# Optimization experiments

Measured on AMD Instinct MI355X. Metric: run time of the kernel, lower is better.

The kernel has to match this reference:

```python
import jax, jax.numpy as jnp
import numpy as np

D_MODEL = 1024
N_HEADS = 16
D_K = D_MODEL // N_HEADS
B, S = 2, 2048


def setup_inputs() -> dict:
    key = jax.random.key(0)
    ks = jax.random.split(key, 5)
    sc = 1.0 / np.sqrt(D_MODEL)
    return {
        "x": jax.random.normal(ks[0], (B, S, D_MODEL), dtype=jnp.float32),
        "W_qkv": jax.random.normal(ks[1], (D_MODEL, 3 * D_MODEL), dtype=jnp.float32) * sc,
        "b_qkv": jnp.zeros((3 * D_MODEL,), dtype=jnp.float32),
        "W_out": jax.random.normal(ks[2], (D_MODEL, D_MODEL), dtype=jnp.float32) * sc,
        "b_out": jnp.zeros((D_MODEL,), dtype=jnp.float32),
    }


def reference(x, W_qkv, b_qkv, W_out, b_out):
    Bb, Ss, _ = x.shape
    qkv = x @ W_qkv + b_qkv                     # [B,S,3*D]
    qkv = qkv.reshape(Bb, Ss, 3, N_HEADS, D_K)
    qkv = jnp.transpose(qkv, (2, 0, 3, 1, 4))   # [3,B,H,S,Dk]
    q, k, v = qkv[0], qkv[1], qkv[2]
    scale = jnp.asarray(np.sqrt(D_K), dtype=x.dtype)
    attn = jnp.einsum('bhsd,bhtd->bhst', q, k) / scale  # [B,H,S,S]
    attn = jax.nn.softmax(attn, axis=-1)
    out = jnp.einsum('bhst,bhtd->bhsd', attn, v)        # [B,H,S,Dk]
    out = jnp.transpose(out, (0, 2, 1, 3)).reshape(Bb, Ss, D_MODEL)
    return out @ W_out + b_out
```

## Files before the change

kernel.cpp:

```cpp
#include <hip/hip_runtime.h>

typedef __bf16 bf16x8 __attribute__((ext_vector_type(8)));
typedef __bf16 bf16x4 __attribute__((ext_vector_type(4)));
typedef float f32x4 __attribute__((ext_vector_type(4)));
typedef unsigned short u16;
typedef unsigned int u32;

__device__ __forceinline__ u16 f2bu(float f) {
  __bf16 h = (__bf16)f;
  return __builtin_bit_cast(u16, h);
}

__device__ __forceinline__ void gld16(const u16* g, const __bf16* lds) {
  __builtin_amdgcn_global_load_lds(
      (const __attribute__((address_space(1))) u32*)(uintptr_t)g,
      (__attribute__((address_space(3))) u32*)(u32)(uintptr_t)lds, 16, 0, 0);
}

__device__ __forceinline__ void tr_tile(const float* __restrict__ in, u16* __restrict__ out,
                                        int R, int C, int bx, int by, int tid) {
  __shared__ u16 t[64][65];
  int tx = tid & 63, ty = tid >> 6;
  int r0 = by * 64, c0 = bx * 64;
  for (int i = 0; i < 16; ++i)
    t[ty + i * 4][tx] = f2bu(in[(size_t)(r0 + ty + i * 4) * C + c0 + tx]);
  __syncthreads();
  for (int i = 0; i < 16; ++i)
    out[(size_t)(c0 + ty + i * 4) * R + r0 + tx] = t[tx][ty + i * 4];
}

__global__ __launch_bounds__(256) void prep(const float* __restrict__ Wqkv,
                                            u16* __restrict__ Wqkv_t,
                                            const float* __restrict__ Wout,
                                            u16* __restrict__ Wout_t,
                                            const float* __restrict__ x,
                                            u16* __restrict__ xb) {
  int id = blockIdx.x, tid = threadIdx.x;
  if (id < 768) {
    tr_tile(Wqkv, Wqkv_t, 1024, 3072, id % 48, id / 48, tid);
  } else if (id < 1024) {
    int id2 = id - 768;
    tr_tile(Wout, Wout_t, 1024, 1024, id2 % 16, id2 / 16, tid);
  } else {
    size_t i = ((size_t)(id - 1024) * 256 + tid) * 8;
    f32x4 a0 = *(const f32x4*)(x + i);
    f32x4 a1 = *(const f32x4*)(x + i + 4);
    bf16x8 v;
    for (int j = 0; j < 4; ++j) { v[j] = (__bf16)a0[j]; v[j + 4] = (__bf16)a1[j]; }
    *(bf16x8*)(xb + i) = v;
  }
}

template <int MODE, int TM>
__global__ __launch_bounds__(256) void gemm_bt(const u16* __restrict__ A,
                                               const u16* __restrict__ Bt,
                                               const float* __restrict__ bias,
                                               void* __restrict__ O0v,
                                               u16* __restrict__ O1,
                                               u16* __restrict__ O2,
                                               int M, int N, int K) {
  constexpr int NI = TM / 32;
  constexpr int AE = TM * 32;
  __shared__ __bf16 smem[2 * AE + 2 * 4096];

  int tid = threadIdx.x;
  int w = tid >> 6, lane = tid & 63, quad = lane >> 4, l16 = lane & 15;
  int wr = w >> 1, wc = w & 1;
  int m0 = blockIdx.y * TM, n0 = blockIdx.x * 128;

  int srow = w * 16 + (lane >> 2);
  int sch = (lane & 3) ^ ((lane >> 3) & 3);
  const u16* Ag = A + (size_t)(m0 + srow) * K + sch * 8;
  const u16* Bg = Bt + (size_t)(n0 + srow) * K + sch * 8;

  int swl = (quad ^ ((l16 >> 1) & 3)) << 3;

  f32x4 acc[NI][4] = {};

  for (int k0 = 0; k0 < K; k0 += 64) {
    __syncthreads();
    for (int s = 0; s < 2; ++s) {
      int kk = k0 + s * 32;
      for (int p = 0; p < TM / 64; ++p)
        gld16(Ag + (size_t)p * 64 * K + kk, smem + s * AE + w * 512 + p * 2048);
      for (int p = 0; p < 2; ++p)
        gld16(Bg + (size_t)p * 64 * K + kk, smem + 2 * AE + s * 4096 + w * 512 + p * 2048);
    }
    __syncthreads();
    for (int s = 0; s < 2; ++s) {
      const __bf16* Asub = smem + s * AE;
      const __bf16* Bsub = smem + 2 * AE + s * 4096;
      bf16x8 af[NI], bfr[4];
      for (int i = 0; i < NI; ++i)
        af[i] = *(const bf16x8*)(Asub + (wr * (TM / 2) + i * 16 + l16) * 32 + swl);
      for (int j = 0; j < 4; ++j)
        bfr[j] = *(const bf16x8*)(Bsub + (wc * 64 + j * 16 + l16) * 32 + swl);
      for (int i = 0; i < NI; ++i)
        for (int j = 0; j < 4; ++j)
          acc[i][j] = __builtin_amdgcn_mfma_f32_16x16x32_bf16(af[i], bfr[j], acc[i][j], 0, 0, 0);
    }
  }

  if (MODE == 0) {
    float* O0 = (float*)O0v;
    for (int j = 0; j < 4; ++j) {
      int n = n0 + wc * 64 + j * 16 + l16;
      float bv = bias[n];
      for (int i = 0; i < NI; ++i) {
        int mb = m0 + wr * (TM / 2) + i * 16 + quad * 4;
        for (int r = 0; r < 4; ++r)
          O0[(size_t)(mb + r) * N + n] = acc[i][j][r] + bv;
      }
    }
  } else {
    u16* O0 = (u16*)O0v;
    for (int j = 0; j < 4; ++j) {
      int n = n0 + wc * 64 + j * 16 + l16;
      int which = n >> 10, rem = n & 1023, h = rem >> 6, d = rem & 63;
      float bv = bias[n];
      for (int i = 0; i < NI; ++i) {
        for (int r = 0; r < 4; ++r) {
          int m = m0 + wr * (TM / 2) + i * 16 + quad * 4 + r;
          int b = m >> 11, s = m & 2047;
          int bhh = b * 16 + h;
          u16 val = f2bu(acc[i][j][r] + bv);
          if (which == 0)
            O0[(((size_t)bhh) * 2048 + s) * 64 + d] = val;
          else if (which == 1)
            O1[(((size_t)bhh) * 2048 + s) * 64 + d] = val;
          else
            O2[((size_t)bhh * 64 + d) * 2048 + s] = val;
        }
      }
    }
  }
}

__global__ __launch_bounds__(256, 4) void flash_attn(const u16* __restrict__ Q,
                                                     const u16* __restrict__ K,
                                                     const u16* __restrict__ Vt,
                                                     u16* __restrict__ AO) {
  constexpr int S = 2048;
  __shared__ __bf16 Ks[2][64 * 64];
  __shared__ __bf16 Vs[2][64 * 64];
  __shared__ __bf16 Ps[4][16 * 64];

  int bh = blockIdx.x, qbase = blockIdx.y * 64;
  int tid = threadIdx.x, w = tid >> 6, lane = tid & 63, quad = lane >> 4, l16 = lane & 15;

  const u16* Qh = Q + (size_t)bh * S * 64;
  const u16* Kh = K + (size_t)bh * S * 64;
  const u16* Vh = Vt + (size_t)bh * 64 * S;

  int qrow = qbase + w * 16 + l16;
  bf16x8 qf0 = *(const bf16x8*)(Qh + (size_t)qrow * 64 + quad * 8);
  bf16x8 qf1 = *(const bf16x8*)(Qh + (size_t)qrow * 64 + 32 + quad * 8);

  int r0s = tid >> 3, b0s = tid & 7;
  int r1s = r0s + 32;
  int ko0 = r0s * 64 + ((b0s ^ (r0s & 7)) << 3);
  int ko1 = r1s * 64 + ((b0s ^ (r1s & 7)) << 3);

  bf16x8 kr0, kr1, vr0, vr1;
#define LOAD_TILE(tb)                                                   \
  {                                                                     \
    kr0 = *(const bf16x8*)(Kh + (size_t)((tb) + r0s) * 64 + b0s * 8);   \
    kr1 = *(const bf16x8*)(Kh + (size_t)((tb) + r1s) * 64 + b0s * 8);   \
    vr0 = *(const bf16x8*)(Vh + (size_t)r0s * S + (tb) + b0s * 8);      \
    vr1 = *(const bf16x8*)(Vh + (size_t)r1s * S + (tb) + b0s * 8);      \
  }
#define STORE_TILE(c)                                                   \
  {                                                                     \
    *(bf16x8*)(&Ks[c][ko0]) = kr0;                                      \
    *(bf16x8*)(&Ks[c][ko1]) = kr1;                                      \
    *(bf16x8*)(&Vs[c][ko0]) = vr0;                                      \
    *(bf16x8*)(&Vs[c][ko1]) = vr1;                                      \
  }

  LOAD_TILE(0);
  STORE_TILE(0);
  LOAD_TILE(64);
  __syncthreads();

  constexpr float C1 = 0.125f * 1.44269504f;
  constexpr float C0 = -12.0f * 1.44269504f;

  f32x4 lsum = {0.f, 0.f, 0.f, 0.f};
  f32x4 o[4] = {};
  int xr = l16 & 7;
  int pw_base = l16 * 64 + (quad & 1) * 4;
  int pw_blk = quad >> 1;

  for (int it = 0; it < S / 64; ++it) {
    int c = it & 1;
    if (it + 1 < S / 64) STORE_TILE(1 - c);
    if (it + 2 < S / 64) LOAD_TILE((it + 2) * 64);

    for (int nt = 0; nt < 4; ++nt) {
      const __bf16* kb = &Ks[c][(nt * 16 + l16) * 64];
      bf16x8 kf0 = *(const bf16x8*)(kb + ((quad ^ xr) << 3));
      bf16x8 kf1 = *(const bf16x8*)(kb + (((quad + 4) ^ xr) << 3));
      f32x4 cc = {0.f, 0.f, 0.f, 0.f};
      cc = __builtin_amdgcn_mfma_f32_16x16x32_bf16(kf0, qf0, cc, 0, 0, 0);
      cc = __builtin_amdgcn_mfma_f32_16x16x32_bf16(kf1, qf1, cc, 0, 0, 0);
      bf16x4 pk;
      for (int r = 0; r < 4; ++r) {
        float p = __builtin_amdgcn_exp2f(fmaf(cc[r], C1, C0));
        lsum[r] += p;
        pk[r] = (__bf16)p;
      }
      *(bf16x4*)(&Ps[w][pw_base + (((nt * 2 + pw_blk) ^ xr) << 3)]) = pk;
    }

    bf16x8 pf0 = *(const bf16x8*)(&Ps[w][l16 * 64 + ((quad ^ xr) << 3)]);
    bf16x8 pf1 = *(const bf16x8*)(&Ps[w][l16 * 64 + (((quad + 4) ^ xr) << 3)]);
    for (int dt = 0; dt < 4; ++dt) {
      const __bf16* vb = &Vs[c][(dt * 16 + l16) * 64];
      bf16x8 v0 = *(const bf16x8*)(vb + ((quad ^ xr) << 3));
      bf16x8 v1 = *(const bf16x8*)(vb + (((quad + 4) ^ xr) << 3));
      o[dt] = __builtin_amdgcn_mfma_f32_16x16x32_bf16(pf0, v0, o[dt], 0, 0, 0);
      o[dt] = __builtin_amdgcn_mfma_f32_16x16x32_bf16(pf1, v1, o[dt], 0, 0, 0);
    }
    __syncthreads();
  }
#undef LOAD_TILE
#undef STORE_TILE

  float l_part = (lsum[0] + lsum[1]) + (lsum[2] + lsum[3]);
  l_part += __shfl_xor(l_part, 16);
  l_part += __shfl_xor(l_part, 32);
  float linv[4];
  for (int r = 0; r < 4; ++r)
    linv[r] = 1.f / __shfl(l_part, quad * 4 + r);

  int b = bh >> 4, h = bh & 15;
  for (int dt = 0; dt < 4; ++dt)
    for (int r = 0; r < 4; ++r) {
      int s = qbase + w * 16 + quad * 4 + r;
      int d = dt * 16 + l16;
      AO[(((size_t)b * 2048 + s) * 16 + h) * 64 + d] = f2bu(o[dt][r] * linv[r]);
    }
}

extern "C" void kernel_launch(void* const* d_in, const int* in_sizes, int n_in,
                              void* d_out, int out_size, void* d_ws, size_t ws_size,
                              hipStream_t stream) {
  const float* x    = (const float*)d_in[0];
  const float* Wqkv = (const float*)d_in[1];
  const float* bqkv = (const float*)d_in[2];
  const float* Wout = (const float*)d_in[3];
  const float* bout = (const float*)d_in[4];
  float* out = (float*)d_out;

  u16* ws = (u16*)d_ws;
  size_t off = 0;
  u16* Wqkv_t = ws + off; off += (size_t)3072 * 1024;
  u16* Wout_t = ws + off; off += (size_t)1024 * 1024;
  u16* xb     = ws + off; off += (size_t)4096 * 1024;
  u16* Qb     = ws + off; off += (size_t)32 * 2048 * 64;
  u16* Kb     = ws + off; off += (size_t)32 * 2048 * 64;
  u16* Vtb    = ws + off; off += (size_t)32 * 2048 * 64;
  u16* AO     = xb;

  prep<<<dim3(3072), 256, 0, stream>>>(Wqkv, Wqkv_t, Wout, Wout_t, x, xb);
  gemm_bt<1, 128><<<dim3(3072 / 128, 4096 / 128), 256, 0, stream>>>(
      xb, Wqkv_t, bqkv, (void*)Qb, Kb, Vtb, 4096, 3072, 1024);
  flash_attn<<<dim3(32, 32), 256, 0, stream>>>(Qb, Kb, Vtb, AO);
  gemm_bt<0, 64><<<dim3(1024 / 128, 4096 / 64), 256, 0, stream>>>(
      AO, Wout_t, bout, (void*)out, nullptr, nullptr, 4096, 1024, 1024);
}
```

Baseline: 213.1 us.

## Write V row-major from QKV GEMM, transpose separately; smaller out-proj N tile

The QKV GEMM epilogue now writes V in the same [bh,s,d] layout as Q and K instead of scattering a transposed store, and a new small kernel transposes V through LDS into the layout flash attention expects. The output projection GEMM also gets a templated N tile and now uses 64x64 tiles, launching more blocks. The aim is to remove the strided V stores and improve occupancy in the final GEMM, at the cost of an extra kernel launch and an extra round trip of V through global memory.

```diff
diff --git a/kernel.cpp b/kernel.cpp
--- a/kernel.cpp
+++ b/kernel.cpp
@@ -51,7 +51,22 @@
   }
 }
 
-template <int MODE, int TM>
+__global__ __launch_bounds__(256) void transpose_v(const u16* __restrict__ V,
+                                                   u16* __restrict__ Vt) {
+  constexpr int S = 2048;
+  __shared__ u16 t[64][65];
+  int bh = blockIdx.y, s0 = blockIdx.x * 64;
+  const u16* in = V + (size_t)bh * S * 64;
+  u16* out = Vt + (size_t)bh * 64 * S;
+  int tx = threadIdx.x & 63, ty = threadIdx.x >> 6;
+  for (int i = 0; i < 16; ++i)
+    t[ty + i * 4][tx] = in[(size_t)(s0 + ty + i * 4) * 64 + tx];
+  __syncthreads();
+  for (int i = 0; i < 16; ++i)
+    out[(size_t)(ty + i * 4) * S + s0 + tx] = t[tx][ty + i * 4];
+}
+
+template <int MODE, int TM, int TN>
 __global__ __launch_bounds__(256) void gemm_bt(const u16* __restrict__ A,
                                                const u16* __restrict__ Bt,
                                                const float* __restrict__ bias,
@@ -60,13 +75,15 @@
                                                u16* __restrict__ O2,
                                                int M, int N, int K) {
   constexpr int NI = TM / 32;
+  constexpr int NJ = TN / 32;
   constexpr int AE = TM * 32;
-  __shared__ __bf16 smem[2 * AE + 2 * 4096];
+  constexpr int BE = TN * 32;
+  __shared__ __bf16 smem[2 * AE + 2 * BE];
 
   int tid = threadIdx.x;
   int w = tid >> 6, lane = tid & 63, quad = lane >> 4, l16 = lane & 15;
   int wr = w >> 1, wc = w & 1;
-  int m0 = blockIdx.y * TM, n0 = blockIdx.x * 128;
+  int m0 = blockIdx.y * TM, n0 = blockIdx.x * TN;
 
   int srow = w * 16 + (lane >> 2);
   int sch = (lane & 3) ^ ((lane >> 3) & 3);
@@ -75,7 +92,7 @@
 
   int swl = (quad ^ ((l16 >> 1) & 3)) << 3;
 
-  f32x4 acc[NI][4] = {};
+  f32x4 acc[NI][NJ] = {};
 
   for (int k0 = 0; k0 < K; k0 += 64) {
     __syncthreads();
@@ -83,28 +100,28 @@
       int kk = k0 + s * 32;
       for (int p = 0; p < TM / 64; ++p)
         gld16(Ag + (size_t)p * 64 * K + kk, smem + s * AE + w * 512 + p * 2048);
-      for (int p = 0; p < 2; ++p)
-        gld16(Bg + (size_t)p * 64 * K + kk, smem + 2 * AE + s * 4096 + w * 512 + p * 2048);
+      for (int p = 0; p < TN / 64; ++p)
+        gld16(Bg + (size_t)p * 64 * K + kk, smem + 2 * AE + s * BE + w * 512 + p * 2048);
     }
     __syncthreads();
     for (int s = 0; s < 2; ++s) {
       const __bf16* Asub = smem + s * AE;
-      const __bf16* Bsub = smem + 2 * AE + s * 4096;
-      bf16x8 af[NI], bfr[4];
+      const __bf16* Bsub = smem + 2 * AE + s * BE;
+      bf16x8 af[NI], bfr[NJ];
       for (int i = 0; i < NI; ++i)
         af[i] = *(const bf16x8*)(Asub + (wr * (TM / 2) + i * 16 + l16) * 32 + swl);
-      for (int j = 0; j < 4; ++j)
-        bfr[j] = *(const bf16x8*)(Bsub + (wc * 64 + j * 16 + l16) * 32 + swl);
+      for (int j = 0; j < NJ; ++j)
+        bfr[j] = *(const bf16x8*)(Bsub + (wc * (TN / 2) + j * 16 + l16) * 32 + swl);
       for (int i = 0; i < NI; ++i)
-        for (int j = 0; j < 4; ++j)
+        for (int j = 0; j < NJ; ++j)
           acc[i][j] = __builtin_amdgcn_mfma_f32_16x16x32_bf16(af[i], bfr[j], acc[i][j], 0, 0, 0);
     }
   }
 
   if (MODE == 0) {
     float* O0 = (float*)O0v;
-    for (int j = 0; j < 4; ++j) {
-      int n = n0 + wc * 64 + j * 16 + l16;
+    for (int j = 0; j < NJ; ++j) {
+      int n = n0 + wc * (TN / 2) + j * 16 + l16;
       float bv = bias[n];
       for (int i = 0; i < NI; ++i) {
         int mb = m0 + wr * (TM / 2) + i * 16 + quad * 4;
@@ -114,22 +131,19 @@
     }
   } else {
     u16* O0 = (u16*)O0v;
-    for (int j = 0; j < 4; ++j) {
-      int n = n0 + wc * 64 + j * 16 + l16;
+    for (int j = 0; j < NJ; ++j) {
+      int n = n0 + wc * (TN / 2) + j * 16 + l16;
       int which = n >> 10, rem = n & 1023, h = rem >> 6, d = rem & 63;
       float bv = bias[n];
       for (int i = 0; i < NI; ++i) {
         for (int r = 0; r < 4; ++r) {
           int m = m0 + wr * (TM / 2) + i * 16 + quad * 4 + r;
           int b = m >> 11, s = m & 2047;
-          int bhh = b * 16 + h;
+          size_t o = (((size_t)(b * 16 + h)) * 2048 + s) * 64 + d;
           u16 val = f2bu(acc[i][j][r] + bv);
-          if (which == 0)
-            O0[(((size_t)bhh) * 2048 + s) * 64 + d] = val;
-          else if (which == 1)
-            O1[(((size_t)bhh) * 2048 + s) * 64 + d] = val;
-          else
-            O2[((size_t)bhh * 64 + d) * 2048 + s] = val;
+          if (which == 0) O0[o] = val;
+          else if (which == 1) O1[o] = val;
+          else O2[o] = val;
         }
       }
     }
@@ -259,13 +273,15 @@
   u16* xb     = ws + off; off += (size_t)4096 * 1024;
   u16* Qb     = ws + off; off += (size_t)32 * 2048 * 64;
   u16* Kb     = ws + off; off += (size_t)32 * 2048 * 64;
+  u16* Vb     = ws + off; off += (size_t)32 * 2048 * 64;
   u16* Vtb    = ws + off; off += (size_t)32 * 2048 * 64;
   u16* AO     = xb;
 
   prep<<<dim3(3072), 256, 0, stream>>>(Wqkv, Wqkv_t, Wout, Wout_t, x, xb);
-  gemm_bt<1, 128><<<dim3(3072 / 128, 4096 / 128), 256, 0, stream>>>(
-      xb, Wqkv_t, bqkv, (void*)Qb, Kb, Vtb, 4096, 3072, 1024);
+  gemm_bt<1, 128, 128><<<dim3(3072 / 128, 4096 / 128), 256, 0, stream>>>(
+      xb, Wqkv_t, bqkv, (void*)Qb, Kb, Vb, 4096, 3072, 1024);
+  transpose_v<<<dim3(32, 32), 256, 0, stream>>>(Vb, Vtb);
   flash_attn<<<dim3(32, 32), 256, 0, stream>>>(Qb, Kb, Vtb, AO);
-  gemm_bt<0, 64><<<dim3(1024 / 128, 4096 / 64), 256, 0, stream>>>(
+  gemm_bt<0, 64, 64><<<dim3(1024 / 64, 4096 / 64), 256, 0, stream>>>(
       AO, Wout_t, bout, (void*)out, nullptr, nullptr, 4096, 1024, 1024);
 }
```

New measurement: 200.8 us. 5.8% less time.
